# Kernel tuning notes

Measured on AMD Instinct MI355X. Metric: run time of the kernel, lower is better.

The kernel has to match this reference:

```python
import jax, jax.numpy as jnp
import numpy as np

B, S, D = 4, 2048, 1024
H, DK, DV = 16, 64, 64

def setup_inputs() -> dict:
    key = jax.random.key(0)
    ks = jax.random.split(key, 8)
    def xavier(k, fan_in, fan_out):
        limit = float(np.sqrt(6.0 / (fan_in + fan_out)))
        return jax.random.uniform(k, (fan_in, fan_out), jnp.float32, -limit, limit)
    return {
        "Q": jax.random.normal(ks[0], (B, S, D), jnp.float32),
        "K": jax.random.normal(ks[1], (B, S, D), jnp.float32),
        "V": jax.random.normal(ks[2], (B, S, D), jnp.float32),
        "mask": jax.random.uniform(ks[3], (B, S), jnp.float32),
        "Wq": xavier(ks[4], D, H * DK),  # stored [in, out]; torch Linear applies x @ W.T
        "bq": jnp.zeros((H * DK,), jnp.float32),
        "Wk": xavier(ks[5], D, H * DK),
        "bk": jnp.zeros((H * DK,), jnp.float32),
        "Wv": xavier(ks[6], D, H * DV),
        "bv": jnp.zeros((H * DV,), jnp.float32),
    }

def reference(Q, K, V, mask, Wq, bq, Wk, bk, Wv, bv):
    b, s, _ = Q.shape
    # projections -> [b, h, s, d]
    q = (Q @ Wq + bq).reshape(b, s, H, DK).transpose(0, 2, 1, 3)
    k = (K @ Wk + bk).reshape(b, s, H, DK).transpose(0, 2, 1, 3)
    v = (V @ Wv + bv).reshape(b, s, H, DV).transpose(0, 2, 1, 3)
    scores = jnp.einsum('bhqd,bhkd->bhqk', q, k) / jnp.sqrt(jnp.float32(DK))
    e = jnp.exp(scores)  # NOTE: raw exp, no max-subtraction (faithful to source)
    e = e * mask[:, None, None, :]  # multiplicative mask over key dim
    attn = e / (jnp.sum(e, axis=-1, keepdims=True) + 1e-8)
    context = jnp.einsum('bhqk,bhkd->bhqd', attn, v)
    return context.transpose(0, 2, 1, 3).reshape(b, s, H * DV)
```

## Files before the change

### kernel.cpp

```cpp
#include <hip/hip_runtime.h>
#include <hip/hip_bf16.h>
#include <stdint.h>

typedef short bf16x8 __attribute__((ext_vector_type(8)));
typedef float f32x4 __attribute__((ext_vector_type(4)));
typedef unsigned int u32x2 __attribute__((ext_vector_type(2)));
typedef unsigned int u32x4 __attribute__((ext_vector_type(4)));

__device__ __forceinline__ unsigned short f2bf(float f) {
  union { float f; unsigned u; } x; x.f = f;
  unsigned r = x.u + 0x7FFFu + ((x.u >> 16) & 1u);
  return (unsigned short)(r >> 16);
}

__device__ __forceinline__ unsigned pk2bf(float a, float b) {
  union { __hip_bfloat162 h; unsigned u; } x;
  x.h = __float22bfloat162_rn(make_float2(a, b));
  return x.u;
}

__device__ __forceinline__ float exp2_fast(float x) {
#if __has_builtin(__builtin_amdgcn_exp2f)
  return __builtin_amdgcn_exp2f(x);
#else
  float r; asm("v_exp_f32 %0, %1" : "=v"(r) : "v"(x)); return r;
#endif
}

typedef const __attribute__((address_space(1))) unsigned int* gptr_t;
typedef __attribute__((address_space(3))) unsigned int* lptr_t;
__device__ __forceinline__ void gll16(const void* g, void* l) {
  __builtin_amdgcn_global_load_lds((gptr_t)g, (lptr_t)l, 16, 0, 0);
}

#define QSCALE 0.18033688011116f

__global__ __launch_bounds__(1024) void wt_kernel(const float* __restrict__ Wq,
                                                  const float* __restrict__ Wk,
                                                  const float* __restrict__ Wv,
                                                  unsigned short* __restrict__ wt) {
  const float* W = blockIdx.z == 0 ? Wq : (blockIdx.z == 1 ? Wk : Wv);
  unsigned short* o = wt + (size_t)blockIdx.z * 1048576;
  __shared__ float t[32][33];
  int tx = threadIdx.x, ty = threadIdx.y;
  t[ty][tx] = W[(size_t)(blockIdx.y * 32 + ty) * 1024 + blockIdx.x * 32 + tx];
  __syncthreads();
  o[(size_t)(blockIdx.x * 32 + ty) * 1024 + blockIdx.y * 32 + tx] = f2bf(t[tx][ty]);
}

__global__ __launch_bounds__(256) void cvt_kernel(const float* __restrict__ Q,
                                                  const float* __restrict__ K,
                                                  const float* __restrict__ V,
                                                  unsigned short* __restrict__ out) {
  int y = blockIdx.y;
  const float* s = y == 0 ? Q : (y == 1 ? K : V);
  unsigned short* o = out + (size_t)y * 8388608;
  size_t idx = ((size_t)blockIdx.x * 256 + threadIdx.x) * 8;
  float4 f0 = *(const float4*)(s + idx);
  float4 f1 = *(const float4*)(s + idx + 4);
  u32x4 r = {pk2bf(f0.x, f0.y), pk2bf(f0.z, f0.w), pk2bf(f1.x, f1.y), pk2bf(f1.z, f1.w)};
  *(u32x4*)(o + idx) = r;
}

__global__ __launch_bounds__(256, 2) void proj_kernel(
    const unsigned short* __restrict__ Xb, const unsigned short* __restrict__ wt,
    const float* __restrict__ bq, const float* __restrict__ bk, const float* __restrict__ bv,
    const float* __restrict__ mask,
    unsigned short* __restrict__ qo, unsigned short* __restrict__ ko, unsigned short* __restrict__ vo) {
  int p = blockIdx.z;
  const unsigned short* X = Xb + (size_t)p * 8388608;
  const unsigned short* Wt = wt + (size_t)p * 1048576;
  const float* bias = p == 0 ? bq : (p == 1 ? bk : bv);
  unsigned short* out = p == 0 ? qo : (p == 1 ? ko : vo);

  __shared__ __align__(16) unsigned short abuf[2][8192];
  __shared__ __align__(16) unsigned short bbuf[2][8192];

  int tid = threadIdx.x;
  int lane = tid & 63, w = tid >> 6;
  int l15 = lane & 15, quad = lane >> 4;
  int wm = w >> 1, wn = w & 1;
  int m0 = blockIdx.x * 128, n0 = blockIdx.y * 128;

  const unsigned short* wsrc[4];
  const unsigned short* xsrc[4];
  for (int j = 0; j < 4; ++j) {
    int stj = w * 4 + j;
    int kt = stj >> 3, t = stj & 7;
    wsrc[j] = Wt + (size_t)(n0 + t * 16 + l15) * 1024 + kt * 32 + quad * 8;
    xsrc[j] = X  + (size_t)(m0 + t * 16 + l15) * 1024 + kt * 32 + quad * 8;
  }

#define PSTAGE(bi, k0)                                        \
  for (int j = 0; j < 4; ++j) {                               \
    gll16(wsrc[j] + (k0), &bbuf[bi][(w * 4 + j) * 512]);      \
    gll16(xsrc[j] + (k0), &abuf[bi][(w * 4 + j) * 512]);      \
  }

  f32x4 acc[4][4] = {};

  PSTAGE(0, 0);
  __syncthreads();

  for (int kk = 0; kk < 16; ++kk) {
    int cur = kk & 1;
    if (kk < 15) PSTAGE(cur ^ 1, (kk + 1) * 64);

    for (int kt = 0; kt < 2; ++kt) {
      bf16x8 af[4], bfr[4];
      for (int i = 0; i < 4; ++i) af[i]  = *(const bf16x8*)&abuf[cur][(kt * 8 + wm * 4 + i) * 512 + lane * 8];
      for (int j = 0; j < 4; ++j) bfr[j] = *(const bf16x8*)&bbuf[cur][(kt * 8 + wn * 4 + j) * 512 + lane * 8];
      for (int i = 0; i < 4; ++i)
        for (int j = 0; j < 4; ++j)
          acc[i][j] = __builtin_amdgcn_mfma_f32_16x16x32_bf16(af[i], bfr[j], acc[i][j], 0, 0, 0);
    }
    __syncthreads();
  }
#undef PSTAGE

  bool isv = (p == 2);
  bool isq = (p == 0);
  for (int j = 0; j < 4; ++j) {
    int n = n0 + wn * 64 + j * 16 + l15;
    float bl = bias[n];
    int h = n >> 6, d = n & 63;
    for (int i = 0; i < 4; ++i) {
      for (int r = 0; r < 4; ++r) {
        int m = m0 + wm * 64 + i * 16 + quad * 4 + r;
        int b = m >> 11, s = m & 2047;
        float val = acc[i][j][r] + bl;
        if (isq) val *= QSCALE;
        if (isv) val *= mask[m];
        size_t idx;
        if (isv) idx = ((size_t)((b * 16 + h) * 64 + d) << 11) + s;
        else     idx = ((size_t)((b * 16 + h) * 2048 + s) << 6) + d;
        out[idx] = f2bf(val);
      }
    }
  }
}

__global__ __launch_bounds__(512, 4) void attn_kernel(
    const unsigned short* __restrict__ q, const unsigned short* __restrict__ k,
    const unsigned short* __restrict__ vT, const float* __restrict__ mask,
    float* __restrict__ out) {
  int qb = blockIdx.x, h = blockIdx.y, b = blockIdx.z;
  int tid = threadIdx.x, lane = tid & 63, w = tid >> 6;
  int l15 = lane & 15, quad = lane >> 4;

  __shared__ __align__(16) unsigned short kbuf[2][4096];
  __shared__ __align__(16) unsigned short vbuf[2][4096];
  __shared__ __align__(16) unsigned short pbuf[8][2048];

  const unsigned short* qp = q + (size_t)(b * 16 + h) * 2048 * 64;
  const unsigned short* kp = k + (size_t)(b * 16 + h) * 2048 * 64;
  const unsigned short* vp = vT + (size_t)(b * 16 + h) * 64 * 2048;
  const float* mp = mask + (size_t)b * 2048;

  bf16x8 aq[2][2];
  for (int nt = 0; nt < 2; ++nt)
    for (int kt = 0; kt < 2; ++kt)
      aq[nt][kt] = *(const bf16x8*)(qp + (size_t)(qb * 256 + w * 32 + nt * 16 + l15) * 64 + kt * 32 + quad * 8);

  f32x4 oacc[2][4] = {};
  f32x4 dacc[2] = {};

  unsigned short* pw = pbuf[w];

  int skt = w >> 2, sm = w & 3;
  const unsigned short* ksrc0 = kp + (size_t)(sm * 16 + l15) * 64 + skt * 32 + quad * 8;
  const unsigned short* vsrc0 = vp + (size_t)(sm * 16 + l15) * 2048 + skt * 32 + quad * 8;

#define STAGE(bi, t)                                    \
  do {                                                  \
    gll16(ksrc0 + (size_t)(t) * 64 * 64, &kbuf[bi][w * 512]); \
    gll16(vsrc0 + (size_t)(t) * 64,      &vbuf[bi][w * 512]); \
  } while (0)

  STAGE(0, 0);
  __syncthreads();

  for (int t = 0; t < 32; ++t) {
    int cur = t & 1;
    if (t + 1 < 32) STAGE(cur ^ 1, t + 1);

    f32x4 sacc[4][2] = {};
    __builtin_amdgcn_s_setprio(1);
    for (int m = 0; m < 4; ++m)
      for (int kt = 0; kt < 2; ++kt) {
        bf16x8 ak = *(const bf16x8*)&kbuf[cur][(kt * 4 + m) * 512 + lane * 8];
        sacc[m][0] = __builtin_amdgcn_mfma_f32_16x16x32_bf16(ak, aq[0][kt], sacc[m][0], 0, 0, 0);
        sacc[m][1] = __builtin_amdgcn_mfma_f32_16x16x32_bf16(ak, aq[1][kt], sacc[m][1], 0, 0, 0);
      }
    __builtin_amdgcn_s_setprio(0);

    for (int m = 0; m < 4; ++m)
      for (int nt = 0; nt < 2; ++nt) {
        float e0 = exp2_fast(sacc[m][nt][0]);
        float e1 = exp2_fast(sacc[m][nt][1]);
        float e2 = exp2_fast(sacc[m][nt][2]);
        float e3 = exp2_fast(sacc[m][nt][3]);
        u32x2 wv = {pk2bf(e0, e1), pk2bf(e2, e3)};
        *(u32x2*)&pw[(nt * 4 + m) * 256 + lane * 4] = wv;
      }

    int kbase = t * 64;
    for (int kt = 0; kt < 2; ++kt) {
      int m = kt * 2 + (quad >> 1);
      int srcl = ((quad & 1) * 2) * 16 + l15;
      bf16x8 pa[2];
      for (int mt = 0; mt < 2; ++mt) {
        union { u32x2 p[2]; bf16x8 v; } u;
        int base = (mt * 4 + m) * 256 + srcl * 4;
        u.p[0] = *(const u32x2*)&pw[base];
        u.p[1] = *(const u32x2*)&pw[base + 64];
        pa[mt] = u.v;
      }
      float4 m0v = *(const float4*)&mp[kbase + kt * 32 + quad * 8];
      float4 m1v = *(const float4*)&mp[kbase + kt * 32 + quad * 8 + 4];
      union { u32x4 u; bf16x8 v; } mu;
      mu.u = (u32x4){pk2bf(m0v.x, m0v.y), pk2bf(m0v.z, m0v.w),
                     pk2bf(m1v.x, m1v.y), pk2bf(m1v.z, m1v.w)};
      __builtin_amdgcn_s_setprio(1);
      dacc[0] = __builtin_amdgcn_mfma_f32_16x16x32_bf16(pa[0], mu.v, dacc[0], 0, 0, 0);
      dacc[1] = __builtin_amdgcn_mfma_f32_16x16x32_bf16(pa[1], mu.v, dacc[1], 0, 0, 0);
      for (int nt = 0; nt < 4; ++nt) {
        bf16x8 bv = *(const bf16x8*)&vbuf[cur][(kt * 4 + nt) * 512 + lane * 8];
        oacc[0][nt] = __builtin_amdgcn_mfma_f32_16x16x32_bf16(pa[0], bv, oacc[0][nt], 0, 0, 0);
        oacc[1][nt] = __builtin_amdgcn_mfma_f32_16x16x32_bf16(pa[1], bv, oacc[1][nt], 0, 0, 0);
      }
      __builtin_amdgcn_s_setprio(0);
    }
    __syncthreads();
  }
#undef STAGE

  for (int mt = 0; mt < 2; ++mt)
    for (int r = 0; r < 4; ++r) {
      int s = qb * 256 + w * 32 + mt * 16 + quad * 4 + r;
      float rden = 1.0f / (dacc[mt][r] + 1e-8f);
      for (int nt = 0; nt < 4; ++nt) {
        int dv = nt * 16 + l15;
        out[(size_t)(b * 2048 + s) * 1024 + h * 64 + dv] = oacc[mt][nt][r] * rden;
      }
    }
}

extern "C" void kernel_launch(void* const* d_in, const int* in_sizes, int n_in,
                              void* d_out, int out_size, void* d_ws, size_t ws_size,
                              hipStream_t stream) {
  const float* Q    = (const float*)d_in[0];
  const float* K    = (const float*)d_in[1];
  const float* V    = (const float*)d_in[2];
  const float* mask = (const float*)d_in[3];
  const float* Wq   = (const float*)d_in[4];
  const float* bq   = (const float*)d_in[5];
  const float* Wk   = (const float*)d_in[6];
  const float* bk   = (const float*)d_in[7];
  const float* Wv   = (const float*)d_in[8];
  const float* bv   = (const float*)d_in[9];

  char* ws = (char*)d_ws;
  unsigned short* wt = (unsigned short*)ws;
  unsigned short* qb = (unsigned short*)(ws + 6291456);
  unsigned short* kb = (unsigned short*)(ws + 23068672);
  unsigned short* vb = (unsigned short*)(ws + 39845888);
  unsigned short* xb = (unsigned short*)(ws + 56623104);

  hipLaunchKernelGGL(wt_kernel, dim3(32, 32, 3), dim3(32, 32), 0, stream, Wq, Wk, Wv, wt);
  hipLaunchKernelGGL(cvt_kernel, dim3(4096, 3), dim3(256), 0, stream, Q, K, V, xb);
  hipLaunchKernelGGL(proj_kernel, dim3(64, 8, 3), dim3(256), 0, stream,
                     xb, wt, bq, bk, bv, mask, qb, kb, vb);
  hipLaunchKernelGGL(attn_kernel, dim3(8, 16, 4), dim3(512), 0, stream,
                     qb, kb, vb, mask, (float*)d_out);
}
```

Baseline: 372.6 us.

## Enlarge projection GEMM tile to 256x128 with 512 threads per block

```diff
diff --git a/kernel.cpp b/kernel.cpp
--- a/kernel.cpp
+++ b/kernel.cpp
@@ -62,7 +62,7 @@
   *(u32x4*)(o + idx) = r;
 }
 
-__global__ __launch_bounds__(256, 2) void proj_kernel(
+__global__ __launch_bounds__(512, 2) void proj_kernel(
     const unsigned short* __restrict__ Xb, const unsigned short* __restrict__ wt,
     const float* __restrict__ bq, const float* __restrict__ bk, const float* __restrict__ bv,
     const float* __restrict__ mask,
@@ -73,29 +73,36 @@
   const float* bias = p == 0 ? bq : (p == 1 ? bk : bv);
   unsigned short* out = p == 0 ? qo : (p == 1 ? ko : vo);
 
-  __shared__ __align__(16) unsigned short abuf[2][8192];
-  __shared__ __align__(16) unsigned short bbuf[2][8192];
+  __shared__ __align__(16) unsigned short sbuf[2][24576];
 
   int tid = threadIdx.x;
   int lane = tid & 63, w = tid >> 6;
   int l15 = lane & 15, quad = lane >> 4;
   int wm = w >> 1, wn = w & 1;
-  int m0 = blockIdx.x * 128, n0 = blockIdx.y * 128;
-
-  const unsigned short* wsrc[4];
-  const unsigned short* xsrc[4];
+  int m0 = blockIdx.x * 256, n0 = blockIdx.y * 128;
+
+  const unsigned short* asrc[4];
+  const unsigned short* bsrc[2];
+#pragma unroll
   for (int j = 0; j < 4; ++j) {
-    int stj = w * 4 + j;
-    int kt = stj >> 3, t = stj & 7;
-    wsrc[j] = Wt + (size_t)(n0 + t * 16 + l15) * 1024 + kt * 32 + quad * 8;
-    xsrc[j] = X  + (size_t)(m0 + t * 16 + l15) * 1024 + kt * 32 + quad * 8;
-  }
-
-#define PSTAGE(bi, k0)                                        \
-  for (int j = 0; j < 4; ++j) {                               \
-    gll16(wsrc[j] + (k0), &bbuf[bi][(w * 4 + j) * 512]);      \
-    gll16(xsrc[j] + (k0), &abuf[bi][(w * 4 + j) * 512]);      \
-  }
+    int stj = w * 4 + j, kt = stj >> 4, t = stj & 15;
+    asrc[j] = X + (size_t)(m0 + t * 16 + l15) * 1024 + kt * 32 + quad * 8;
+  }
+#pragma unroll
+  for (int j = 0; j < 2; ++j) {
+    int sbj = w * 2 + j, kt = sbj >> 3, t = sbj & 7;
+    bsrc[j] = Wt + (size_t)(n0 + t * 16 + l15) * 1024 + kt * 32 + quad * 8;
+  }
+
+#define PSTAGE(bi, k0)                                                 \
+  do {                                                                 \
+    _Pragma("unroll")                                                  \
+    for (int j = 0; j < 4; ++j)                                        \
+      gll16(asrc[j] + (k0), &sbuf[bi][8192 + (w * 4 + j) * 512]);      \
+    _Pragma("unroll")                                                  \
+    for (int j = 0; j < 2; ++j)                                        \
+      gll16(bsrc[j] + (k0), &sbuf[bi][(w * 2 + j) * 512]);             \
+  } while (0)
 
   f32x4 acc[4][4] = {};
 
@@ -106,11 +113,18 @@
     int cur = kk & 1;
     if (kk < 15) PSTAGE(cur ^ 1, (kk + 1) * 64);
 
+#pragma unroll
     for (int kt = 0; kt < 2; ++kt) {
       bf16x8 af[4], bfr[4];
-      for (int i = 0; i < 4; ++i) af[i]  = *(const bf16x8*)&abuf[cur][(kt * 8 + wm * 4 + i) * 512 + lane * 8];
-      for (int j = 0; j < 4; ++j) bfr[j] = *(const bf16x8*)&bbuf[cur][(kt * 8 + wn * 4 + j) * 512 + lane * 8];
+#pragma unroll
       for (int i = 0; i < 4; ++i)
+        af[i] = *(const bf16x8*)&sbuf[cur][8192 + (kt * 16 + wm * 4 + i) * 512 + lane * 8];
+#pragma unroll
+      for (int j = 0; j < 4; ++j)
+        bfr[j] = *(const bf16x8*)&sbuf[cur][(kt * 8 + wn * 4 + j) * 512 + lane * 8];
+#pragma unroll
+      for (int i = 0; i < 4; ++i)
+#pragma unroll
         for (int j = 0; j < 4; ++j)
           acc[i][j] = __builtin_amdgcn_mfma_f32_16x16x32_bf16(af[i], bfr[j], acc[i][j], 0, 0, 0);
     }
@@ -269,7 +283,7 @@
 
   hipLaunchKernelGGL(wt_kernel, dim3(32, 32, 3), dim3(32, 32), 0, stream, Wq, Wk, Wv, wt);
   hipLaunchKernelGGL(cvt_kernel, dim3(4096, 3), dim3(256), 0, stream, Q, K, V, xb);
-  hipLaunchKernelGGL(proj_kernel, dim3(64, 8, 3), dim3(256), 0, stream,
+  hipLaunchKernelGGL(proj_kernel, dim3(32, 8, 3), dim3(512), 0, stream,
                      xb, wt, bq, bk, bv, mask, qb, kb, vb);
   hipLaunchKernelGGL(attn_kernel, dim3(8, 16, 4), dim3(512), 0, stream,
                      qb, kb, vb, mask, (float*)d_out);
```

Result: no change. 370.9 us (-0.5%).
